# Performance work log

Measured on AMD Instinct MI355X. Metric: run time of the kernel, lower is better.

The kernel has to match this reference:

```python
import jax, jax.numpy as jnp
import numpy as np

NX, NY = 256, 256            # img_size
NUM_DET, VIEW = 368, 180
SDD, SCD = 1000.0, 500.0
DCD = SDD - SCD
DET_INT = 2.0
PX = 1.0                     # pixel_size
SHIFT = 0.0                  # no quarter offset


def _geometry():
    # Faithful numpy port of FP.param_setting (equally_spaced mode)
    d_beta = np.pi * 360.0 / VIEW / 180.0
    beta = np.linspace(0.0, (VIEW - 1) * d_beta, VIEW)
    axis_x = np.linspace(-NX / 2, NX / 2, NX + 1) * PX          # [NX+1]
    axis_y = np.linspace(-NY / 2, NY / 2, NY + 1) * PX          # [NY+1]
    range_det_x = np.ones(NUM_DET) * DCD
    range_det_y = np.linspace(-(NUM_DET - 1) / 2, (NUM_DET - 1) / 2, NUM_DET) * DET_INT + SHIFT
    src = np.array([-SCD, 0.0])
    cb, sb = np.cos(beta), np.sin(beta)
    src_point = np.stack([src[0] * cb + src[1] * sb, -src[0] * sb + src[1] * cb])  # [2, V]
    det_x_rot = cb[None, :] * range_det_x[:, None] + sb[None, :] * range_det_y[:, None]   # [D, V]
    det_y_rot = -sb[None, :] * range_det_x[:, None] + cb[None, :] * range_det_y[:, None]  # [D, V]
    ax = (axis_x[:, None] - src_point[0][None, :])[None, :, :] / (det_x_rot - src_point[0])[:, None, :]  # [D, NX+1, V]
    ay = (axis_y[:, None] - src_point[1][None, :])[None, :, :] / (det_y_rot - src_point[1])[:, None, :]  # [D, NY+1, V]
    a_min = np.maximum(np.minimum(ax[:, 0, :], ax[:, -1, :]), np.minimum(ay[:, 0, :], ay[:, -1, :]))
    a_min[a_min < 0] = 0.0
    a_max = np.minimum(np.maximum(ax[:, 0, :], ax[:, -1, :]), np.maximum(ay[:, 0, :], ay[:, -1, :]))
    a_max[a_max > 1] = 1.0
    axy = np.concatenate([ax, ay], axis=1)                       # [D, NX+NY+2, V]
    axy[(axy > a_max[:, None, :]) | (axy < a_min[:, None, :])] = np.nan
    axy = np.sort(axy, axis=1)                                   # NaNs sort to the end (matches torch)
    diff_axy = np.diff(axy, n=1, axis=1)                         # [D, S, V], S = NX+NY+1
    a_mid = axy[:, :-1, :] + diff_axy / 2
    diff_axy = np.nan_to_num(diff_axy, nan=0.0)
    a_mid = np.nan_to_num(a_mid, nan=0.0)
    s2d = np.sqrt((det_x_rot - src_point[0]) ** 2 + (det_y_rot - src_point[1]) ** 2)  # [D, V]
    weighting = diff_axy.transpose(0, 2, 1)[None, None] * s2d[None, None, :, :, None]  # [1,1,D,V,S]
    x_pos = a_mid * (det_x_rot[:, None, :] - src_point[0]) + src_point[0]
    x_pos = x_pos.transpose(0, 2, 1) / (PX * (NX - 1) / 2)       # [D, V, S]
    y_pos = a_mid * (det_y_rot[:, None, :] - src_point[1]) + src_point[1]
    y_pos = y_pos.transpose(0, 2, 1) / (PX * (NY - 1) / 2)
    grid_pos = np.stack([x_pos, y_pos], axis=-1)                 # [D, V, S, 2]
    return grid_pos.astype(np.float32), weighting.astype(np.float32)


def _bilinear_sample(img, gx, gy):
    # torch.nn.functional.grid_sample: bilinear, padding_mode='zeros', align_corners=False
    # img: [B,C,H,W]; gx indexes W, gy indexes H; gx/gy: [D,V,S]
    B, C, H, W = img.shape
    ix = ((gx + 1.0) * W - 1.0) * 0.5
    iy = ((gy + 1.0) * H - 1.0) * 0.5
    ix0 = jnp.floor(ix)
    iy0 = jnp.floor(iy)
    wx1 = ix - ix0
    wy1 = iy - iy0
    out = jnp.zeros((B, C) + gx.shape, dtype=img.dtype)
    for dx in (0, 1):
        for dy in (0, 1):
            xi = ix0 + dx
            yi = iy0 + dy
            w = (wx1 if dx else 1.0 - wx1) * (wy1 if dy else 1.0 - wy1)
            valid = (xi >= 0) & (xi < W) & (yi >= 0) & (yi < H)
            xi_c = jnp.clip(xi, 0, W - 1).astype(jnp.int32)
            yi_c = jnp.clip(yi, 0, H - 1).astype(jnp.int32)
            out = out + img[:, :, yi_c, xi_c] * (w * valid)[None, None]
    return out  # [B,C,D,V,S]


def setup_inputs() -> dict:
    key = jax.random.key(0)
    img = jax.random.normal(key, (1, 1, NX, NY), dtype=jnp.float32)
    gp, wt = _geometry()
    return {"img": img, "grid_pos": jnp.asarray(gp), "weighting": jnp.asarray(wt)}


def reference(img, grid_pos, weighting):
    # All views vectorized at once (torch version loops over views)
    interp = _bilinear_sample(img, grid_pos[..., 0], grid_pos[..., 1])  # [B,C,D,V,S]
    sino = jnp.sum(weighting * interp, axis=-1)                         # [B,C,D,V]
    return jnp.where(jnp.isnan(sino), jnp.zeros((), sino.dtype), sino)
```

## Files before the change

kernel.cpp:

```cpp
#include <hip/hip_runtime.h>
#include <hip/hip_fp16.h>
#include <math.h>


constexpr int IMG_N  = 256;
constexpr int NDET   = 368;
constexpr int NVIEW  = 180;
constexpr int NSAMP  = 2 * IMG_N + 1;
constexpr int DV     = NDET * NVIEW;
constexpr int NITER  = (NSAMP + 63) / 64;
constexpr int PN     = IMG_N + 1;

struct __align__(8) Corner { __half2 ab; __half2 cd; };

constexpr size_t PACK_BYTES = (size_t)PN * PN * sizeof(Corner);
constexpr size_t RT_OFF     = (PACK_BYTES + 255) & ~(size_t)255;
constexpr size_t RT_BYTES   = (size_t)DV * 3 * sizeof(float4);
constexpr size_t KR_OFF     = RT_OFF + RT_BYTES;
constexpr size_t KR_BYTES   = (size_t)DV * sizeof(int2);
constexpr size_t WS_NEEDED  = KR_OFF + KR_BYTES;

constexpr int PACK_BLOCKS = (PN * PN + 255) / 256;
constexpr int GEOM_BLOCKS = (DV + 255) / 256;

__device__ __forceinline__ double valAP(double A, double s, double inv, int k) {
    return (A + s * (double)k) * inv;
}

__global__ __launch_bounds__(256) void prep_kernel(
    const float* __restrict__ img, Corner* __restrict__ P2,
    float4* __restrict__ rt, int2* __restrict__ kr)
{
    const int b = blockIdx.x;
    if (b < PACK_BLOCKS) {
        const int idx = b * 256 + threadIdx.x;
        if (idx >= PN * PN) return;
        const int yi = idx / PN;
        const int xi = idx - yi * PN;
        const int y0 = yi - 1, x0 = xi - 1;
        float v[2][2];
        #pragma unroll
        for (int dy = 0; dy < 2; ++dy)
            #pragma unroll
            for (int dx = 0; dx < 2; ++dx) {
                const int y = y0 + dy, x = x0 + dx;
                v[dy][dx] = (((unsigned)y) < 256u && ((unsigned)x) < 256u)
                          ? img[y * IMG_N + x] : 0.0f;
            }
        Corner c;
        c.ab = __floats2half2_rn(v[0][0], v[0][1]);
        c.cd = __floats2half2_rn(v[1][0], v[1][1]);
        P2[idx] = c;
        return;
    }

    const int idx = (b - PACK_BLOCKS) * 256 + threadIdx.x;
    if (idx >= DV) return;
    const int d = idx / NVIEW;
    const int v = idx - d * NVIEW;

    const double d_beta = ((M_PI * 360.0) / (double)NVIEW) / 180.0;
    const double stop   = (double)(NVIEW - 1) * d_beta;
    const double step   = stop / (double)(NVIEW - 1);
    const double beta   = (v == NVIEW - 1) ? stop : (double)v * step;
    const double cb = cos(beta), sb = sin(beta);

    const double sx  = -500.0 * cb;
    const double sy  =  500.0 * sb;
    const double rdy = ((double)d - 183.5) * 2.0;
    const double dx  = cb * 500.0 + sb * rdy;
    const double dy  = (-sb) * 500.0 + cb * rdy;
    const double ddx = dx - sx, ddy = dy - sy;

    double Ax, sxn;
    const double invx = 1.0 / ddx;
    if (invx >= 0.0) { Ax = -128.0 - sx; sxn = 1.0; }
    else             { Ax =  128.0 - sx; sxn = -1.0; }
    double Ay, syn;
    const double invy = 1.0 / ddy;
    if (invy >= 0.0) { Ay = -128.0 - sy; syn = 1.0; }
    else             { Ay =  128.0 - sy; syn = -1.0; }

    const double vx0 = valAP(Ax, sxn, invx, 0), vxN = valAP(Ax, sxn, invx, IMG_N);
    const double vy0 = valAP(Ay, syn, invy, 0), vyN = valAP(Ay, syn, invy, IMG_N);
    double a_min = fmax(vx0, vy0); if (a_min < 0.0) a_min = 0.0;
    double a_max = fmin(vxN, vyN); if (a_max > 1.0) a_max = 1.0;

    const double absdx = fabs(ddx), absdy = fabs(ddy);

    int klox, khix, kloy, khiy;
    {
        double kd = (a_min - vx0) * absdx;
        kd = fmin(fmax(kd, -1.0), 258.0);
        int k = (int)kd; k = max(0, min(k, 256));
        while (k > 0    && valAP(Ax, sxn, invx, k - 1) >= a_min) --k;
        while (k <= 256 && valAP(Ax, sxn, invx, k) < a_min)      ++k;
        klox = k;
        kd = (a_max - vx0) * absdx;
        kd = fmin(fmax(kd, -1.0), 258.0);
        k = (int)kd; k = max(0, min(k, 256));
        while (k > 0    && valAP(Ax, sxn, invx, k - 1) > a_max)  --k;
        while (k <= 256 && valAP(Ax, sxn, invx, k) <= a_max)     ++k;
        khix = k - 1;
        if (klox > khix) { klox = 0; khix = -1; }
    }
    {
        double kd = (a_min - vy0) * absdy;
        kd = fmin(fmax(kd, -1.0), 258.0);
        int k = (int)kd; k = max(0, min(k, 256));
        while (k > 0    && valAP(Ay, syn, invy, k - 1) >= a_min) --k;
        while (k <= 256 && valAP(Ay, syn, invy, k) < a_min)      ++k;
        kloy = k;
        kd = (a_max - vy0) * absdy;
        kd = fmin(fmax(kd, -1.0), 258.0);
        k = (int)kd; k = max(0, min(k, 256));
        while (k > 0    && valAP(Ay, syn, invy, k - 1) > a_max)  --k;
        while (k <= 256 && valAP(Ay, syn, invy, k) <= a_max)     ++k;
        khiy = k - 1;
        if (kloy > khiy) { kloy = 0; khiy = -1; }
    }

    const int nx = khix - klox + 1;
    const int ny = khiy - kloy + 1;
    const double s2d = sqrt(ddx * ddx + ddy * ddy);

    const double sxd = sxn * invx, syd = syn * invy;
    const double bxd = (Ax + sxn * (double)klox) * invx;
    const double byd = (Ay + syn * (double)kloy) * invy;
    const double ssum = sxd + syd;
    const double c0 = (byd - bxd) / ssum;
    const double c1 = syd / ssum;

    float4* o = rt + (size_t)idx * 3;
    o[0] = make_float4((float)bxd, (float)sxd, (float)byd, (float)syd);
    o[1] = make_float4((float)c0, (float)c1, (float)s2d, 0.0f);
    o[2] = make_float4((float)(ddx * (128.0 / 127.5)),
                       (float)(sx  * (128.0 / 127.5) + 127.5),
                       (float)(ddy * (128.0 / 127.5)),
                       (float)(sy  * (128.0 / 127.5) + 127.5));
    kr[idx] = make_int2(nx, ny);
}

__global__ __launch_bounds__(256) void fp_siddon(
    const Corner* __restrict__ P2,
    const float4* __restrict__ rt,
    const int2*   __restrict__ kr,
    float*        __restrict__ out)
{
    const int wave = threadIdx.x >> 6;
    const int lane = threadIdx.x & 63;
    const int dv   = __builtin_amdgcn_readfirstlane(blockIdx.x * 4 + wave);

    const float4 A = rt[(size_t)dv * 3 + 0];
    const float4 B = rt[(size_t)dv * 3 + 1];
    const float4 C = rt[(size_t)dv * 3 + 2];
    const int2 nn = kr[dv];
    const int nx = nn.x, ny = nn.y;
    const int M = nx + ny;
    const int npairs = M - 1;

    float acc = 0.0f;

    for (int base = 0; base < npairs; base += 64) {
        const int p = base + lane;
        const bool act = (p < npairs);
        const int q = act ? p + 1 : 1;
        const int t = q + 1;

        const int mlo = max(0, t - ny);
        const int mhi = min(nx, t);
        int m = (int)fmaf((float)q, B.y, B.x);
        m = max(mlo, min(m, mhi));
        while (m > mlo) {
            const int mm = m - 1;
            const bool Pmm = (t - 1 - mm < 0) || (mm >= nx) ||
                (fmaf((float)(t - 1 - mm), A.w, A.z) <= fmaf((float)mm, A.y, A.x));
            if (!Pmm) break;
            m = mm;
        }
        while (m < mhi) {
            const bool Pm = (t - 1 - m < 0) || (m >= nx) ||
                (fmaf((float)(t - 1 - m), A.w, A.z) <= fmaf((float)m, A.y, A.x));
            if (Pm) break;
            ++m;
        }

        const float xl  = (m > 0)     ? fmaf((float)(m - 1),     A.y, A.x) : -3.0e38f;
        const float yl  = (t - m > 0) ? fmaf((float)(t - 1 - m), A.w, A.z) : -3.0e38f;
        const float cur = fmaxf(xl, yl);
        const float xl2 = (m > 1)     ? fmaf((float)(m - 2),     A.y, A.x) : -3.0e38f;
        const float yl2 = (t - m > 1) ? fmaf((float)(t - 2 - m), A.w, A.z) : -3.0e38f;
        const float prev = (xl >= yl) ? fmaxf(xl2, yl) : fmaxf(xl, yl2);

        const float diff = cur - prev;
        const float mid  = fmaf(diff, 0.5f, prev);
        const float ixp  = fmaf(mid, C.x, C.y);
        const float iyp  = fmaf(mid, C.z, C.w);
        const float wf   = act ? diff * B.z : 0.0f;

        const float fx0 = floorf(ixp), fy0 = floorf(iyp);
        const float wx1 = ixp - fx0,  wy1 = iyp - fy0;
        const int x0 = (int)fx0, y0 = (int)fy0;

        unsigned pidx = (unsigned)(y0 * PN + x0 + (PN + 1));
        pidx = min(pidx, (unsigned)(PN * PN - 1));
        const Corner pc = P2[pidx];
        const float2 r0 = __half22float2(pc.ab);
        const float2 r1 = __half22float2(pc.cd);

        const float wx0 = 1.0f - wx1;
        const float wy0 = 1.0f - wy1;
        const float interp = (r0.x * wx0 + r0.y * wx1) * wy0
                           + (r1.x * wx0 + r1.y * wx1) * wy1;

        acc = fmaf(wf, interp, acc);
    }

    #pragma unroll
    for (int off = 32; off > 0; off >>= 1)
        acc += __shfl_down(acc, off, 64);
    if (lane == 0)
        out[dv] = isnan(acc) ? 0.0f : acc;
}

__global__ __launch_bounds__(256) void fp_kernel_nopack(
    const float*  __restrict__ img,
    const float2* __restrict__ grid,
    const float*  __restrict__ wt,
    float*        __restrict__ out)
{
    const int wave = threadIdx.x >> 6;
    const int lane = threadIdx.x & 63;
    const int dv   = blockIdx.x * 4 + wave;
    const long base = (long)dv * NSAMP;

    float2 g[NITER];
    float  w[NITER];
    #pragma unroll
    for (int k = 0; k < NITER; ++k) {
        const int s = lane + k * 64;
        if (s < NSAMP) { g[k] = grid[base + s]; w[k] = wt[base + s]; }
        else           { g[k] = make_float2(0.0f, 0.0f); w[k] = 0.0f; }
    }
    float acc = 0.0f;
    #pragma unroll
    for (int k = 0; k < NITER; ++k) {
        const float ix = ((g[k].x + 1.0f) * 256.0f - 1.0f) * 0.5f;
        const float iy = ((g[k].y + 1.0f) * 256.0f - 1.0f) * 0.5f;
        const float fx0 = floorf(ix), fy0 = floorf(iy);
        const float wx1 = ix - fx0,  wy1 = iy - fy0;
        const int x0 = (int)fx0, y0 = (int)fy0;
        const int xc  = min(max(x0, 0), IMG_N - 2);
        const int yc0 = min(max(y0, 0), IMG_N - 1);
        const int yc1 = min(max(y0 + 1, 0), IMG_N - 1);
        const float2 p0 = *(const float2*)(img + yc0 * IMG_N + xc);
        const float2 p1 = *(const float2*)(img + yc1 * IMG_N + xc);
        const bool x0v = ((unsigned)x0) < 256u;
        const bool x1v = ((unsigned)(x0 + 1)) < 256u;
        const bool hiX = (x0 == IMG_N - 1);
        const bool loX = (x0 == -1);
        const float v00 = x0v ? (hiX ? p0.y : p0.x) : 0.0f;
        const float v01 = x1v ? (loX ? p0.x : p0.y) : 0.0f;
        const float v10 = x0v ? (hiX ? p1.y : p1.x) : 0.0f;
        const float v11 = x1v ? (loX ? p1.x : p1.y) : 0.0f;
        const float my0 = (((unsigned)y0) < 256u) ? 1.0f : 0.0f;
        const float my1 = (((unsigned)(y0 + 1)) < 256u) ? 1.0f : 0.0f;
        const float wx0 = 1.0f - wx1;
        const float wy0 = (1.0f - wy1) * my0;
        const float wy1m = wy1 * my1;
        acc += w[k] * ((v00 * wx0 + v01 * wx1) * wy0
                     + (v10 * wx0 + v11 * wx1) * wy1m);
    }
    #pragma unroll
    for (int off = 32; off > 0; off >>= 1)
        acc += __shfl_down(acc, off, 64);
    if (lane == 0) out[dv] = isnan(acc) ? 0.0f : acc;
}

extern "C" void kernel_launch(void* const* d_in, const int* in_sizes, int n_in,
                              void* d_out, int out_size, void* d_ws, size_t ws_size,
                              hipStream_t stream) {
    const float*  img  = (const float*)d_in[0];
    const float2* grid = (const float2*)d_in[1];
    const float*  wt   = (const float*)d_in[2];
    float*        out  = (float*)d_out;

    if (ws_size >= WS_NEEDED) {
        Corner* P2 = (Corner*)d_ws;
        float4* rt = (float4*)((char*)d_ws + RT_OFF);
        int2*   kr = (int2*)  ((char*)d_ws + KR_OFF);
        prep_kernel<<<PACK_BLOCKS + GEOM_BLOCKS, 256, 0, stream>>>(img, P2, rt, kr);
        fp_siddon<<<DV / 4, 256, 0, stream>>>(P2, rt, kr, out);
    } else {
        fp_kernel_nopack<<<DV / 4, 256, 0, stream>>>(img, grid, wt, out);
    }
}
```

Before: 395.2 us.

## Enumerate Siddon segments per dominant-axis cell with transposed corner table

Replaces the per-segment merge search (binary-like walk to find the m-th crossing) with a per-cell enumeration along the axis with fewer crossings. Each lane handles one such cell and emits up to three segments from the other axis's crossings. A transposed packed corner table is built so swapped-axis rays can reuse the same gather code. This cuts the while-loop search work per sample, at the cost of more prep work, a second packed image buffer and up to three gathers per lane.

```diff
diff --git a/kernel.cpp b/kernel.cpp
--- a/kernel.cpp
+++ b/kernel.cpp
@@ -14,10 +14,11 @@
 struct __align__(8) Corner { __half2 ab; __half2 cd; };
 
 constexpr size_t PACK_BYTES = (size_t)PN * PN * sizeof(Corner);
-constexpr size_t RT_OFF     = (PACK_BYTES + 255) & ~(size_t)255;
+constexpr size_t PT_OFF     = (PACK_BYTES + 255) & ~(size_t)255;
+constexpr size_t RT_OFF     = (PT_OFF + PACK_BYTES + 255) & ~(size_t)255;
 constexpr size_t RT_BYTES   = (size_t)DV * 3 * sizeof(float4);
 constexpr size_t KR_OFF     = RT_OFF + RT_BYTES;
-constexpr size_t KR_BYTES   = (size_t)DV * sizeof(int2);
+constexpr size_t KR_BYTES   = (size_t)DV * sizeof(int4);
 constexpr size_t WS_NEEDED  = KR_OFF + KR_BYTES;
 
 constexpr int PACK_BLOCKS = (PN * PN + 255) / 256;
@@ -29,15 +30,17 @@
 
 __global__ __launch_bounds__(256) void prep_kernel(
     const float* __restrict__ img, Corner* __restrict__ P2,
-    float4* __restrict__ rt, int2* __restrict__ kr)
+    Corner* __restrict__ PT2, float4* __restrict__ rt, int4* __restrict__ kr)
 {
     const int b = blockIdx.x;
-    if (b < PACK_BLOCKS) {
-        const int idx = b * 256 + threadIdx.x;
+    if (b < 2 * PACK_BLOCKS) {
+        const bool tr = (b >= PACK_BLOCKS);
+        const int idx = (tr ? b - PACK_BLOCKS : b) * 256 + threadIdx.x;
         if (idx >= PN * PN) return;
-        const int yi = idx / PN;
-        const int xi = idx - yi * PN;
-        const int y0 = yi - 1, x0 = xi - 1;
+        const int oi = idx / PN;
+        const int ii = idx - oi * PN;
+        const int y0 = (tr ? ii : oi) - 1;
+        const int x0 = (tr ? oi : ii) - 1;
         float v[2][2];
         #pragma unroll
         for (int dy = 0; dy < 2; ++dy)
@@ -48,13 +51,19 @@
                           ? img[y * IMG_N + x] : 0.0f;
             }
         Corner c;
-        c.ab = __floats2half2_rn(v[0][0], v[0][1]);
-        c.cd = __floats2half2_rn(v[1][0], v[1][1]);
-        P2[idx] = c;
+        if (!tr) {
+            c.ab = __floats2half2_rn(v[0][0], v[0][1]);
+            c.cd = __floats2half2_rn(v[1][0], v[1][1]);
+            P2[idx] = c;
+        } else {
+            c.ab = __floats2half2_rn(v[0][0], v[1][0]);
+            c.cd = __floats2half2_rn(v[0][1], v[1][1]);
+            PT2[idx] = c;
+        }
         return;
     }
 
-    const int idx = (b - PACK_BLOCKS) * 256 + threadIdx.x;
+    const int idx = (b - 2 * PACK_BLOCKS) * 256 + threadIdx.x;
     if (idx >= DV) return;
     const int d = idx / NVIEW;
     const int v = idx - d * NVIEW;
@@ -120,31 +129,64 @@
         if (kloy > khiy) { kloy = 0; khiy = -1; }
     }
 
-    const int nx = khix - klox + 1;
-    const int ny = khiy - kloy + 1;
+    int nx = khix - klox + 1;
+    int ny = khiy - kloy + 1;
     const double s2d = sqrt(ddx * ddx + ddy * ddy);
 
-    const double sxd = sxn * invx, syd = syn * invy;
-    const double bxd = (Ax + sxn * (double)klox) * invx;
-    const double byd = (Ay + syn * (double)kloy) * invy;
-    const double ssum = sxd + syd;
-    const double c0 = (byd - bxd) / ssum;
-    const double c1 = syd / ssum;
+    double sxd = sxn * invx, syd = syn * invy;
+    double bxd = (Ax + sxn * (double)klox) * invx;
+    double byd = (Ay + syn * (double)kloy) * invy;
+
+    double cxa = ddx * (128.0 / 127.5), cxb = sx * (128.0 / 127.5) + 127.5;
+    double cya = ddy * (128.0 / 127.5), cyb = sy * (128.0 / 127.5) + 127.5;
+
+    int fl = 0;
+    if (sxd > syd) {
+        double t;
+        t = bxd; bxd = byd; byd = t;
+        t = sxd; sxd = syd; syd = t;
+        int ti = nx; nx = ny; ny = ti;
+        t = cxa; cxa = cya; cya = t;
+        t = cxb; cxb = cyb; cyb = t;
+        fl = 1;
+    }
 
     float4* o = rt + (size_t)idx * 3;
     o[0] = make_float4((float)bxd, (float)sxd, (float)byd, (float)syd);
-    o[1] = make_float4((float)c0, (float)c1, (float)s2d, 0.0f);
-    o[2] = make_float4((float)(ddx * (128.0 / 127.5)),
-                       (float)(sx  * (128.0 / 127.5) + 127.5),
-                       (float)(ddy * (128.0 / 127.5)),
-                       (float)(sy  * (128.0 / 127.5) + 127.5));
-    kr[idx] = make_int2(nx, ny);
+    o[1] = make_float4((float)(1.0 / syd), 0.0f, (float)s2d, 0.0f);
+    o[2] = make_float4((float)cxa, (float)cxb, (float)cya, (float)cyb);
+    kr[idx] = make_int4(nx, ny, fl, 0);
+}
+
+__device__ __forceinline__ float seg(float cur, float nxt, bool valid,
+                                     const float4 C, const float s2d,
+                                     const Corner* __restrict__ T)
+{
+    nxt = valid ? nxt : cur;
+    const float diff = nxt - cur;
+    const float mid  = fmaf(diff, 0.5f, cur);
+    const float wfv  = valid ? diff * s2d : 0.0f;
+    const float ip   = fmaf(mid, C.x, C.y);
+    const float op   = fmaf(mid, C.z, C.w);
+    const float fi = floorf(ip), fo = floorf(op);
+    const float wi1 = ip - fi,  wo1 = op - fo;
+    const int i0 = (int)fi, o0 = (int)fo;
+    unsigned pidx = (unsigned)(o0 * PN + i0 + (PN + 1));
+    pidx = min(pidx, (unsigned)(PN * PN - 1));
+    const Corner pc = T[pidx];
+    const float2 r0 = __half22float2(pc.ab);
+    const float2 r1 = __half22float2(pc.cd);
+    const float wi0 = 1.0f - wi1, wo0 = 1.0f - wo1;
+    const float interp = (r0.x * wi0 + r0.y * wi1) * wo0
+                       + (r1.x * wi0 + r1.y * wi1) * wo1;
+    return wfv * interp;
 }
 
 __global__ __launch_bounds__(256) void fp_siddon(
     const Corner* __restrict__ P2,
+    const Corner* __restrict__ PT2,
     const float4* __restrict__ rt,
-    const int2*   __restrict__ kr,
+    const int4*   __restrict__ kr,
     float*        __restrict__ out)
 {
     const int wave = threadIdx.x >> 6;
@@ -154,66 +196,46 @@
     const float4 A = rt[(size_t)dv * 3 + 0];
     const float4 B = rt[(size_t)dv * 3 + 1];
     const float4 C = rt[(size_t)dv * 3 + 2];
-    const int2 nn = kr[dv];
-    const int nx = nn.x, ny = nn.y;
-    const int M = nx + ny;
-    const int npairs = M - 1;
+    const int4 kk = kr[dv];
+    const int nx = kk.x, ny = kk.y;
+    const Corner* __restrict__ T = kk.z ? PT2 : P2;
 
     float acc = 0.0f;
 
-    for (int base = 0; base < npairs; base += 64) {
-        const int p = base + lane;
-        const bool act = (p < npairs);
-        const int q = act ? p + 1 : 1;
-        const int t = q + 1;
-
-        const int mlo = max(0, t - ny);
-        const int mhi = min(nx, t);
-        int m = (int)fmaf((float)q, B.y, B.x);
-        m = max(mlo, min(m, mhi));
-        while (m > mlo) {
-            const int mm = m - 1;
-            const bool Pmm = (t - 1 - mm < 0) || (mm >= nx) ||
-                (fmaf((float)(t - 1 - mm), A.w, A.z) <= fmaf((float)mm, A.y, A.x));
-            if (!Pmm) break;
-            m = mm;
+    for (int base = 0; base <= nx; base += 64) {
+        const int c = base + lane;
+        const bool act = (c <= nx);
+        const int cc = act ? c : nx;
+        const bool leftEx  = act && (cc >= 1);
+        const bool rightEx = (cc < nx);
+        const float left  = fmaf((float)(cc - 1), A.y, A.x);
+        const float right = fmaf((float)cc,       A.y, A.x);
+
+        int k = 0;
+        if (cc > 0) {
+            k = (int)((left - A.z) * B.x) + 1;
+            k = max(0, min(k, ny));
+            while (k > 0  && fmaf((float)(k - 1), A.w, A.z) >= left) --k;
+            while (k < ny && fmaf((float)k,       A.w, A.z) <  left) ++k;
         }
-        while (m < mhi) {
-            const bool Pm = (t - 1 - m < 0) || (m >= nx) ||
-                (fmaf((float)(t - 1 - m), A.w, A.z) <= fmaf((float)m, A.y, A.x));
-            if (Pm) break;
-            ++m;
-        }
-
-        const float xl  = (m > 0)     ? fmaf((float)(m - 1),     A.y, A.x) : -3.0e38f;
-        const float yl  = (t - m > 0) ? fmaf((float)(t - 1 - m), A.w, A.z) : -3.0e38f;
-        const float cur = fmaxf(xl, yl);
-        const float xl2 = (m > 1)     ? fmaf((float)(m - 2),     A.y, A.x) : -3.0e38f;
-        const float yl2 = (t - m > 1) ? fmaf((float)(t - 2 - m), A.w, A.z) : -3.0e38f;
-        const float prev = (xl >= yl) ? fmaxf(xl2, yl) : fmaxf(xl, yl2);
-
-        const float diff = cur - prev;
-        const float mid  = fmaf(diff, 0.5f, prev);
-        const float ixp  = fmaf(mid, C.x, C.y);
-        const float iyp  = fmaf(mid, C.z, C.w);
-        const float wf   = act ? diff * B.z : 0.0f;
-
-        const float fx0 = floorf(ixp), fy0 = floorf(iyp);
-        const float wx1 = ixp - fx0,  wy1 = iyp - fy0;
-        const int x0 = (int)fx0, y0 = (int)fy0;
-
-        unsigned pidx = (unsigned)(y0 * PN + x0 + (PN + 1));
-        pidx = min(pidx, (unsigned)(PN * PN - 1));
-        const Corner pc = P2[pidx];
-        const float2 r0 = __half22float2(pc.ab);
-        const float2 r1 = __half22float2(pc.cd);
-
-        const float wx0 = 1.0f - wx1;
-        const float wy0 = 1.0f - wy1;
-        const float interp = (r0.x * wx0 + r0.y * wx1) * wy0
-                           + (r1.x * wx0 + r1.y * wx1) * wy1;
-
-        acc = fmaf(wf, interp, acc);
+        const float yk  = fmaf((float)k, A.w, A.z);
+        const bool yIn  = (k < ny) && (!rightEx || yk < right);
+        const float yk1 = fmaf((float)(k + 1), A.w, A.z);
+        const bool y2   = yIn && (k + 1 < ny) && (!rightEx || yk1 < right);
+
+        const bool  e1Ex = yIn || rightEx;
+        const float e1   = yIn ? yk : right;
+        const bool  e2Ex = yIn && (y2 || rightEx);
+        const float e2   = y2 ? yk1 : right;
+
+        const bool vA = leftEx && e1Ex;
+        const bool vB = act && e2Ex;
+        const bool vC = act && y2 && rightEx;
+
+        acc += seg(left, e1, vA, C, B.z, T);
+        acc += seg(e1,   e2, vB, C, B.z, T);
+        if (__any(vC))
+            acc += seg(e2, right, vC, C, B.z, T);
     }
 
     #pragma unroll
@@ -286,11 +308,13 @@
     float*        out  = (float*)d_out;
 
     if (ws_size >= WS_NEEDED) {
-        Corner* P2 = (Corner*)d_ws;
-        float4* rt = (float4*)((char*)d_ws + RT_OFF);
-        int2*   kr = (int2*)  ((char*)d_ws + KR_OFF);
-        prep_kernel<<<PACK_BLOCKS + GEOM_BLOCKS, 256, 0, stream>>>(img, P2, rt, kr);
-        fp_siddon<<<DV / 4, 256, 0, stream>>>(P2, rt, kr, out);
+        Corner* P2  = (Corner*)d_ws;
+        Corner* PT2 = (Corner*)((char*)d_ws + PT_OFF);
+        float4* rt  = (float4*)((char*)d_ws + RT_OFF);
+        int4*   kr  = (int4*)  ((char*)d_ws + KR_OFF);
+        prep_kernel<<<2 * PACK_BLOCKS + GEOM_BLOCKS, 256, 0, stream>>>(
+            img, P2, PT2, rt, kr);
+        fp_siddon<<<DV / 4, 256, 0, stream>>>(P2, PT2, rt, kr, out);
     } else {
         fp_kernel_nopack<<<DV / 4, 256, 0, stream>>>(img, grid, wt, out);
     }
```

After: 413.8 us. 4.7% more time.

## Process two Siddon segments per lane to amortize merge-position search

Applied to the files above, without the earlier changes.

Each lane now handles two consecutive ray segments per iteration. It locates the merge position once and derives three consecutive sorted crossing values, which yield both segments. This halves the per-segment binary-style search and loop overhead, at the cost of more registers and select logic. It also halves the number of active lanes per wave-iteration, which may reduce latency hiding for the gather loads.

```diff
diff --git a/kernel.cpp b/kernel.cpp
--- a/kernel.cpp
+++ b/kernel.cpp
@@ -141,6 +141,30 @@
     kr[idx] = make_int2(nx, ny);
 }
 
+__device__ __forceinline__ float seg(float cur, float nxt, bool valid,
+                                     const float4 C, const float s2d,
+                                     const Corner* __restrict__ T)
+{
+    nxt = valid ? nxt : cur;
+    const float diff = nxt - cur;
+    const float mid  = fmaf(diff, 0.5f, cur);
+    const float wfv  = valid ? diff * s2d : 0.0f;
+    const float ip   = fmaf(mid, C.x, C.y);
+    const float op   = fmaf(mid, C.z, C.w);
+    const float fi = floorf(ip), fo = floorf(op);
+    const float wi1 = ip - fi,  wo1 = op - fo;
+    const int i0 = (int)fi, o0 = (int)fo;
+    unsigned pidx = (unsigned)(o0 * PN + i0 + (PN + 1));
+    pidx = min(pidx, (unsigned)(PN * PN - 1));
+    const Corner pc = T[pidx];
+    const float2 r0 = __half22float2(pc.ab);
+    const float2 r1 = __half22float2(pc.cd);
+    const float wi0 = 1.0f - wi1, wo0 = 1.0f - wo1;
+    const float interp = (r0.x * wi0 + r0.y * wi1) * wo0
+                       + (r1.x * wi0 + r1.y * wi1) * wo1;
+    return wfv * interp;
+}
+
 __global__ __launch_bounds__(256) void fp_siddon(
     const Corner* __restrict__ P2,
     const float4* __restrict__ rt,
@@ -161,59 +185,52 @@
 
     float acc = 0.0f;
 
-    for (int base = 0; base < npairs; base += 64) {
-        const int p = base + lane;
-        const bool act = (p < npairs);
-        const int q = act ? p + 1 : 1;
-        const int t = q + 1;
-
-        const int mlo = max(0, t - ny);
-        const int mhi = min(nx, t);
-        int m = (int)fmaf((float)q, B.y, B.x);
+    for (int base = 0; base < npairs; base += 128) {
+        const int p0 = base + (lane << 1);
+        const bool act1 = (p0 < npairs);
+        const bool act2 = (p0 + 1 < npairs);
+        const int p  = act1 ? p0 : (npairs - 1);
+        const int tp = p + 2 + (act2 ? 1 : 0);
+
+        const int mlo = max(0, tp - ny);
+        const int mhi = min(nx, tp);
+        int m = (int)fmaf((float)(tp - 1), B.y, B.x);
         m = max(mlo, min(m, mhi));
         while (m > mlo) {
             const int mm = m - 1;
-            const bool Pmm = (t - 1 - mm < 0) || (mm >= nx) ||
-                (fmaf((float)(t - 1 - mm), A.w, A.z) <= fmaf((float)mm, A.y, A.x));
+            const bool Pmm = (tp - 1 - mm < 0) || (mm >= nx) ||
+                (fmaf((float)(tp - 1 - mm), A.w, A.z) <= fmaf((float)mm, A.y, A.x));
             if (!Pmm) break;
             m = mm;
         }
         while (m < mhi) {
-            const bool Pm = (t - 1 - m < 0) || (m >= nx) ||
-                (fmaf((float)(t - 1 - m), A.w, A.z) <= fmaf((float)m, A.y, A.x));
+            const bool Pm = (tp - 1 - m < 0) || (m >= nx) ||
+                (fmaf((float)(tp - 1 - m), A.w, A.z) <= fmaf((float)m, A.y, A.x));
             if (Pm) break;
             ++m;
         }
 
-        const float xl  = (m > 0)     ? fmaf((float)(m - 1),     A.y, A.x) : -3.0e38f;
-        const float yl  = (t - m > 0) ? fmaf((float)(t - 1 - m), A.w, A.z) : -3.0e38f;
-        const float cur = fmaxf(xl, yl);
-        const float xl2 = (m > 1)     ? fmaf((float)(m - 2),     A.y, A.x) : -3.0e38f;
-        const float yl2 = (t - m > 1) ? fmaf((float)(t - 2 - m), A.w, A.z) : -3.0e38f;
-        const float prev = (xl >= yl) ? fmaxf(xl2, yl) : fmaxf(xl, yl2);
-
-        const float diff = cur - prev;
-        const float mid  = fmaf(diff, 0.5f, prev);
-        const float ixp  = fmaf(mid, C.x, C.y);
-        const float iyp  = fmaf(mid, C.z, C.w);
-        const float wf   = act ? diff * B.z : 0.0f;
-
-        const float fx0 = floorf(ixp), fy0 = floorf(iyp);
-        const float wx1 = ixp - fx0,  wy1 = iyp - fy0;
-        const int x0 = (int)fx0, y0 = (int)fy0;
-
-        unsigned pidx = (unsigned)(y0 * PN + x0 + (PN + 1));
-        pidx = min(pidx, (unsigned)(PN * PN - 1));
-        const Corner pc = P2[pidx];
-        const float2 r0 = __half22float2(pc.ab);
-        const float2 r1 = __half22float2(pc.cd);
-
-        const float wx0 = 1.0f - wx1;
-        const float wy0 = 1.0f - wy1;
-        const float interp = (r0.x * wx0 + r0.y * wx1) * wy0
-                           + (r1.x * wx0 + r1.y * wx1) * wy1;
-
-        acc = fmaf(wf, interp, acc);
+        const float xl  = (m > 0)      ? fmaf((float)(m - 1),      A.y, A.x) : -3.0e38f;
+        const float xl2 = (m > 1)      ? fmaf((float)(m - 2),      A.y, A.x) : -3.0e38f;
+        const float xl3 = (m > 2)      ? fmaf((float)(m - 3),      A.y, A.x) : -3.0e38f;
+        const float yl  = (tp - m > 0) ? fmaf((float)(tp - 1 - m), A.w, A.z) : -3.0e38f;
+        const float yl2 = (tp - m > 1) ? fmaf((float)(tp - 2 - m), A.w, A.z) : -3.0e38f;
+        const float yl3 = (tp - m > 2) ? fmaf((float)(tp - 3 - m), A.w, A.z) : -3.0e38f;
+
+        const bool xge = (xl >= yl);
+        const float top1 = fmaxf(xl, yl);
+        const float c2 = xge ? xl2 : xl;
+        const float d2 = xge ? yl  : yl2;
+        const bool x2ge = (c2 >= d2);
+        const float top2 = fmaxf(c2, d2);
+        const float xh3 = x2ge ? (xge ? xl3 : xl2) : (xge ? xl2 : xl);
+        const float yh3 = x2ge ? (xge ? yl  : yl2) : (xge ? yl2 : yl3);
+        const float top3 = fmaxf(xh3, yh3);
+
+        const float sA0 = act2 ? top3 : top2;
+        const float sA1 = act2 ? top2 : top1;
+        acc += seg(sA0,  sA1,  act1, C, B.z, P2);
+        acc += seg(top2, top1, act2, C, B.z, P2);
     }
 
     #pragma unroll
```

New measurement: 389.4 us. About the same (-1.5%).
